# Kernel tuning notes

Measured on AMD Instinct MI355X. Metric: run time of the kernel, lower is better.

## Reference

```python
import jax, jax.numpy as jnp
import numpy as np

EPS = 1e-12  # F.normalize default eps

def _l2_normalize(v):
    # torch.nn.functional.normalize: v / max(||v||_2, eps)
    n = jnp.sqrt(jnp.sum(v * v, axis=-1, keepdims=True))
    return v / jnp.maximum(n, EPS)

def setup_inputs() -> dict:
    key = jax.random.key(0)
    k1, k2 = jax.random.split(key)
    B, M, D = 4096, 12893, 2048
    x = jax.random.normal(k1, (B, D), dtype=jnp.float32)
    prototypes = jax.random.normal(k2, (M, D), dtype=jnp.float32)
    distance_scale = jnp.ones((1,), dtype=jnp.float32)
    return {"x": x, "prototypes": prototypes, "distance_scale": distance_scale}

def reference(x, prototypes, distance_scale):
    xn = _l2_normalize(x)            # [B, D]
    pn = _l2_normalize(prototypes)   # [M, D]
    # pairwise Euclidean distance via ||a||^2 + ||b||^2 - 2 a.b (stable clamp)
    xs = jnp.sum(xn * xn, axis=-1, keepdims=True)        # [B, 1]
    ps = jnp.sum(pn * pn, axis=-1)[None, :]              # [1, M]
    d2 = xs + ps - 2.0 * jnp.einsum('bd,md->bm', xn, pn)  # [B, M]
    dist = jnp.sqrt(jnp.maximum(d2, 0.0))
    x3 = -jnp.abs(distance_scale[0]) * dist              # [B, M]
    # original forward returns (x3, x3, x3, x3); all identical
    return x3
```

## Files before the change

kernel.cpp:

```cpp
#include <hip/hip_runtime.h>
#include <hip/hip_bf16.h>
#include <cstdint>
#include <cstddef>

constexpr int BROWS = 4096;
constexpr int MREAL = 12893;
constexpr int MPAD  = 12928;
constexpr int KDIM  = 2048;

typedef __attribute__((ext_vector_type(8))) short short8;
typedef __attribute__((ext_vector_type(4))) float f32x4;

__device__ __forceinline__ void gld_lds16(const void* g, void* l) {
  __builtin_amdgcn_global_load_lds((__attribute__((address_space(1))) const void*)g,
                                   (__attribute__((address_space(3))) void*)l,
                                   16, 0, 0);
}

__global__ void l2norm_bf16(const float* __restrict__ in,
                            __hip_bfloat16* __restrict__ out,
                            int nvalid) {
  const int row = blockIdx.x;
  const int t   = threadIdx.x;
  __hip_bfloat16* orow = out + (size_t)row * KDIM;

  if (row >= nvalid) {
    reinterpret_cast<float4*>(orow)[t] = make_float4(0.f, 0.f, 0.f, 0.f);
    return;
  }

  const float4* irow = reinterpret_cast<const float4*>(in + (size_t)row * KDIM);
  float4 a = irow[t];
  float4 b = irow[t + 256];
  float ss = a.x*a.x + a.y*a.y + a.z*a.z + a.w*a.w
           + b.x*b.x + b.y*b.y + b.z*b.z + b.w*b.w;

  #pragma unroll
  for (int off = 32; off > 0; off >>= 1) ss += __shfl_down(ss, off);

  __shared__ float red[4];
  if ((t & 63) == 0) red[t >> 6] = ss;
  __syncthreads();
  float tot = red[0] + red[1] + red[2] + red[3];
  float inv = 1.0f / fmaxf(sqrtf(tot), 1e-12f);

  union { ushort4 u; __hip_bfloat16 h[4]; } o1, o2;
  o1.h[0] = __float2bfloat16(a.x * inv);
  o1.h[1] = __float2bfloat16(a.y * inv);
  o1.h[2] = __float2bfloat16(a.z * inv);
  o1.h[3] = __float2bfloat16(a.w * inv);
  o2.h[0] = __float2bfloat16(b.x * inv);
  o2.h[1] = __float2bfloat16(b.y * inv);
  o2.h[2] = __float2bfloat16(b.z * inv);
  o2.h[3] = __float2bfloat16(b.w * inv);
  reinterpret_cast<ushort4*>(orow)[t]       = o1.u;
  reinterpret_cast<ushort4*>(orow)[t + 256] = o2.u;
}

__global__ void gemm_dist(const __hip_bfloat16* __restrict__ A,
                          const __hip_bfloat16* __restrict__ P,
                          const float* __restrict__ scale,
                          float* __restrict__ out) {
  __shared__ __hip_bfloat16 sA[128][32];
  __shared__ __hip_bfloat16 sB[128][32];

  const int tid  = threadIdx.x;
  const int lane = tid & 63;
  const int wave = tid >> 6;
  const int wm   = wave >> 1;
  const int wn   = wave & 1;
  const int bm0  = blockIdx.y * 128;
  const int bn0  = blockIdx.x * 128;

  f32x4 acc[4][4];
  #pragma unroll
  for (int i = 0; i < 4; i++)
    #pragma unroll
    for (int j = 0; j < 4; j++)
      acc[i][j] = f32x4{0.f, 0.f, 0.f, 0.f};

  const int sr = tid >> 2;
  const int sc = (tid & 3) << 3;

  const int frow = lane & 15;
  const int koff = (lane >> 4) << 3;

  for (int kt = 0; kt < KDIM; kt += 32) {
    __syncthreads();
    gld_lds16(A + (size_t)(bm0 + sr)      * KDIM + kt + sc, &sA[sr][sc]);
    gld_lds16(A + (size_t)(bm0 + sr + 64) * KDIM + kt + sc, &sA[sr + 64][sc]);
    gld_lds16(P + (size_t)(bn0 + sr)      * KDIM + kt + sc, &sB[sr][sc]);
    gld_lds16(P + (size_t)(bn0 + sr + 64) * KDIM + kt + sc, &sB[sr + 64][sc]);
    __syncthreads();

    short8 af[4], bf[4];
    #pragma unroll
    for (int i = 0; i < 4; i++)
      af[i] = *reinterpret_cast<const short8*>(&sA[wm * 64 + i * 16 + frow][koff]);
    #pragma unroll
    for (int j = 0; j < 4; j++)
      bf[j] = *reinterpret_cast<const short8*>(&sB[wn * 64 + j * 16 + frow][koff]);

    #pragma unroll
    for (int i = 0; i < 4; i++)
      #pragma unroll
      for (int j = 0; j < 4; j++)
        acc[i][j] = __builtin_amdgcn_mfma_f32_16x16x32_bf16(af[i], bf[j],
                                                            acc[i][j], 0, 0, 0);
  }

  const float s = fabsf(scale[0]);
  const int colb = bn0 + wn * 64 + (lane & 15);
  #pragma unroll
  for (int i = 0; i < 4; i++) {
    const int rowb = bm0 + wm * 64 + i * 16 + ((lane >> 4) << 2);
    #pragma unroll
    for (int j = 0; j < 4; j++) {
      const int col = colb + j * 16;
      if (col < MREAL) {
        #pragma unroll
        for (int r = 0; r < 4; r++) {
          float d2 = fmaxf(2.0f - 2.0f * acc[i][j][r], 0.0f);
          out[(size_t)(rowb + r) * MREAL + col] = -s * __builtin_sqrtf(d2);
        }
      }
    }
  }
}

extern "C" void kernel_launch(void* const* d_in, const int* in_sizes, int n_in,
                              void* d_out, int out_size, void* d_ws, size_t ws_size,
                              hipStream_t stream) {
  const float* x = (const float*)d_in[0];
  const float* p = (const float*)d_in[1];
  const float* s = (const float*)d_in[2];
  float* out = (float*)d_out;

  __hip_bfloat16* xn = (__hip_bfloat16*)d_ws;
  __hip_bfloat16* pn = xn + (size_t)BROWS * KDIM;

  l2norm_bf16<<<BROWS, 256, 0, stream>>>(x, xn, BROWS);
  l2norm_bf16<<<MPAD,  256, 0, stream>>>(p, pn, MREAL);

  dim3 grid(MPAD / 128, BROWS / 128);
  gemm_dist<<<grid, 256, 0, stream>>>(xn, pn, s, out);
}
```

Measured before the change: 635.8 us.

## Rewrite GEMM with 256x256 tiles, double-buffered swizzled LDS pipeline, fused normalization

The GEMM now uses 512-thread blocks computing 256x256 output tiles with a K-step of 64. Operands go through double-buffered, XOR-swizzled LDS fed by async global-to-LDS loads, staged across four sub-phases per tile with explicit waitcnt, barriers and setprio. Blocks are remapped with an XCD-aware swizzle over a 1D grid, and the two normalization launches are merged into one. This aims to cut LDS and global traffic per FLOP and to hide load latency, in exchange for much higher register and LDS pressure and a fragile hand-written schedule.

```diff
diff --git a/kernel.cpp b/kernel.cpp
--- a/kernel.cpp
+++ b/kernel.cpp
@@ -7,6 +7,7 @@
 constexpr int MREAL = 12893;
 constexpr int MPAD  = 12928;
 constexpr int KDIM  = 2048;
+constexpr int NT    = KDIM / 64;
 
 typedef __attribute__((ext_vector_type(8))) short short8;
 typedef __attribute__((ext_vector_type(4))) float f32x4;
@@ -17,23 +18,32 @@
                                    16, 0, 0);
 }
 
-__global__ void l2norm_bf16(const float* __restrict__ in,
-                            __hip_bfloat16* __restrict__ out,
-                            int nvalid) {
-  const int row = blockIdx.x;
-  const int t   = threadIdx.x;
-  __hip_bfloat16* orow = out + (size_t)row * KDIM;
-
-  if (row >= nvalid) {
-    reinterpret_cast<float4*>(orow)[t] = make_float4(0.f, 0.f, 0.f, 0.f);
-    return;
-  }
-
-  const float4* irow = reinterpret_cast<const float4*>(in + (size_t)row * KDIM);
-  float4 a = irow[t];
-  float4 b = irow[t + 256];
+__global__ void l2norm_fused(const float* __restrict__ x,
+                             const float* __restrict__ p,
+                             __hip_bfloat16* __restrict__ xn,
+                             __hip_bfloat16* __restrict__ pn) {
+  const int b = blockIdx.x;
+  const int t = threadIdx.x;
+  const float* irow;
+  __hip_bfloat16* orow;
+  if (b < BROWS) {
+    irow = x + (size_t)b * KDIM;
+    orow = xn + (size_t)b * KDIM;
+  } else {
+    const int row = b - BROWS;
+    orow = pn + (size_t)row * KDIM;
+    if (row >= MREAL) {
+      reinterpret_cast<float4*>(orow)[t] = make_float4(0.f, 0.f, 0.f, 0.f);
+      return;
+    }
+    irow = p + (size_t)row * KDIM;
+  }
+
+  const float4* iv = reinterpret_cast<const float4*>(irow);
+  float4 a = iv[t];
+  float4 c = iv[t + 256];
   float ss = a.x*a.x + a.y*a.y + a.z*a.z + a.w*a.w
-           + b.x*b.x + b.y*b.y + b.z*b.z + b.w*b.w;
+           + c.x*c.x + c.y*c.y + c.z*c.z + c.w*c.w;
 
   #pragma unroll
   for (int off = 32; off > 0; off >>= 1) ss += __shfl_down(ss, off);
@@ -49,84 +59,142 @@
   o1.h[1] = __float2bfloat16(a.y * inv);
   o1.h[2] = __float2bfloat16(a.z * inv);
   o1.h[3] = __float2bfloat16(a.w * inv);
-  o2.h[0] = __float2bfloat16(b.x * inv);
-  o2.h[1] = __float2bfloat16(b.y * inv);
-  o2.h[2] = __float2bfloat16(b.z * inv);
-  o2.h[3] = __float2bfloat16(b.w * inv);
+  o2.h[0] = __float2bfloat16(c.x * inv);
+  o2.h[1] = __float2bfloat16(c.y * inv);
+  o2.h[2] = __float2bfloat16(c.z * inv);
+  o2.h[3] = __float2bfloat16(c.w * inv);
   reinterpret_cast<ushort4*>(orow)[t]       = o1.u;
   reinterpret_cast<ushort4*>(orow)[t + 256] = o2.u;
 }
 
-__global__ void gemm_dist(const __hip_bfloat16* __restrict__ A,
-                          const __hip_bfloat16* __restrict__ P,
-                          const float* __restrict__ scale,
-                          float* __restrict__ out) {
-  __shared__ __hip_bfloat16 sA[128][32];
-  __shared__ __hip_bfloat16 sB[128][32];
-
-  const int tid  = threadIdx.x;
-  const int lane = tid & 63;
-  const int wave = tid >> 6;
-  const int wm   = wave >> 1;
-  const int wn   = wave & 1;
-  const int bm0  = blockIdx.y * 128;
-  const int bn0  = blockIdx.x * 128;
-
-  f32x4 acc[4][4];
-  #pragma unroll
-  for (int i = 0; i < 4; i++)
+__global__ __launch_bounds__(512, 2)
+void gemm_dist(const __hip_bfloat16* __restrict__ A,
+               const __hip_bfloat16* __restrict__ P,
+               const float* __restrict__ scale,
+               float* __restrict__ out) {
+  __shared__ __hip_bfloat16 lds[65536];
+  __hip_bfloat16* const sA = lds;
+  __hip_bfloat16* const sB = lds + 32768;
+
+  const int t    = threadIdx.x;
+  const int lane = t & 63;
+  const int wv   = t >> 6;
+  const int wm   = wv >> 2;
+  const int wn   = wv & 3;
+
+  const int bid = blockIdx.x;
+  const int swz = (bid & 7) * 102 + (bid >> 3);
+  const int bm0 = (swz / 51) * 256;
+  const int bn0 = (swz % 51) * 256;
+
+  const int srow = t >> 3;
+  const int sp   = t & 7;
+  const int ssl  = sp ^ (srow & 7);
+  const __hip_bfloat16* aSrc[4];
+  const __hip_bfloat16* bSrc[4];
+  int sOff[4];
+  #pragma unroll
+  for (int r = 0; r < 4; ++r) {
+    aSrc[r] = A + (size_t)(bm0 + r*64 + srow) * KDIM + ssl*8;
+    int br = bn0 + r*64 + srow;
+    br = br < MPAD ? br : (MPAD - 1);
+    bSrc[r] = P + (size_t)br * KDIM + ssl*8;
+    sOff[r] = (r*64 + srow)*64 + sp*8;
+  }
+
+  const int l15 = lane & 15, hi = lane >> 4;
+  const int pk0 = ( hi      ^ (lane & 7)) * 8;
+  const int pk1 = ((hi + 4) ^ (lane & 7)) * 8;
+  const int aBase = (wm*128 + l15) * 64;
+  const int bBase = (wn*64  + l15) * 64;
+
+  f32x4 acc[8][4];
+  #pragma unroll
+  for (int i = 0; i < 8; ++i)
     #pragma unroll
-    for (int j = 0; j < 4; j++)
-      acc[i][j] = f32x4{0.f, 0.f, 0.f, 0.f};
-
-  const int sr = tid >> 2;
-  const int sc = (tid & 3) << 3;
-
-  const int frow = lane & 15;
-  const int koff = (lane >> 4) << 3;
-
-  for (int kt = 0; kt < KDIM; kt += 32) {
-    __syncthreads();
-    gld_lds16(A + (size_t)(bm0 + sr)      * KDIM + kt + sc, &sA[sr][sc]);
-    gld_lds16(A + (size_t)(bm0 + sr + 64) * KDIM + kt + sc, &sA[sr + 64][sc]);
-    gld_lds16(P + (size_t)(bn0 + sr)      * KDIM + kt + sc, &sB[sr][sc]);
-    gld_lds16(P + (size_t)(bn0 + sr + 64) * KDIM + kt + sc, &sB[sr + 64][sc]);
-    __syncthreads();
-
-    short8 af[4], bf[4];
+    for (int j = 0; j < 4; ++j) acc[i][j] = f32x4{0.f, 0.f, 0.f, 0.f};
+
+#define STG_A(BUF, R, T) do { const int kt_ = ((T)*64) & (KDIM-1);            \
+    gld_lds16(aSrc[(R)]   + kt_, sA + (BUF)*16384 + sOff[(R)]);               \
+    gld_lds16(aSrc[(R)+1] + kt_, sA + (BUF)*16384 + sOff[(R)+1]); } while(0)
+#define STG_B(BUF, R, T) do { const int kt_ = ((T)*64) & (KDIM-1);            \
+    gld_lds16(bSrc[(R)]   + kt_, sB + (BUF)*16384 + sOff[(R)]);               \
+    gld_lds16(bSrc[(R)+1] + kt_, sB + (BUF)*16384 + sOff[(R)+1]); } while(0)
+
+  STG_A(0, 0, 0); STG_A(0, 2, 0);
+  STG_B(0, 0, 0); STG_B(0, 2, 0);
+  STG_B(1, 0, 1); STG_B(1, 2, 1);
+  asm volatile("s_waitcnt vmcnt(4)" ::: "memory");
+  __builtin_amdgcn_s_barrier();
+
+  short8 bfr[4][2];
+
+#define PHASE(BUF, Q, READB, STG, VM) do {                                    \
+    asm volatile("" ::: "memory");                                            \
+    const __hip_bfloat16* sAb = sA + (BUF)*16384;                             \
+    const __hip_bfloat16* sBb = sB + (BUF)*16384;                             \
+    if (READB) {                                                              \
+      _Pragma("unroll")                                                       \
+      for (int j = 0; j < 4; ++j) {                                           \
+        bfr[j][0] = *reinterpret_cast<const short8*>(sBb + bBase + j*1024 + pk0); \
+        bfr[j][1] = *reinterpret_cast<const short8*>(sBb + bBase + j*1024 + pk1); \
+      }                                                                       \
+    }                                                                         \
+    const short8 a00 = *reinterpret_cast<const short8*>(sAb + aBase + (Q)*2048 + pk0); \
+    const short8 a01 = *reinterpret_cast<const short8*>(sAb + aBase + (Q)*2048 + pk1); \
+    const short8 a10 = *reinterpret_cast<const short8*>(sAb + aBase + (Q)*2048 + 1024 + pk0); \
+    const short8 a11 = *reinterpret_cast<const short8*>(sAb + aBase + (Q)*2048 + 1024 + pk1); \
+    STG;                                                                      \
+    __builtin_amdgcn_s_barrier();                                             \
+    asm volatile("s_waitcnt lgkmcnt(0)" ::: "memory");                        \
+    __builtin_amdgcn_s_setprio(1);                                            \
+    _Pragma("unroll")                                                         \
+    for (int j = 0; j < 4; ++j) {                                             \
+      acc[2*(Q)  ][j] = __builtin_amdgcn_mfma_f32_16x16x32_bf16(a00, bfr[j][0], acc[2*(Q)  ][j], 0, 0, 0); \
+      acc[2*(Q)  ][j] = __builtin_amdgcn_mfma_f32_16x16x32_bf16(a01, bfr[j][1], acc[2*(Q)  ][j], 0, 0, 0); \
+      acc[2*(Q)+1][j] = __builtin_amdgcn_mfma_f32_16x16x32_bf16(a10, bfr[j][0], acc[2*(Q)+1][j], 0, 0, 0); \
+      acc[2*(Q)+1][j] = __builtin_amdgcn_mfma_f32_16x16x32_bf16(a11, bfr[j][1], acc[2*(Q)+1][j], 0, 0, 0); \
+    }                                                                         \
+    __builtin_amdgcn_s_setprio(0);                                            \
+    if (VM) asm volatile("s_waitcnt vmcnt(4)" ::: "memory");                  \
+    __builtin_amdgcn_s_barrier();                                             \
+  } while (0)
+
+  for (int it = 0; it < NT/2; ++it) {
+    const int T1 = 2*it + 1;
+    PHASE(0, 0, true , STG_A(1, 0, T1),     false);
+    PHASE(0, 1, false, STG_A(1, 2, T1),     false);
+    PHASE(0, 2, false, STG_B(0, 0, (T1+1)), false);
+    PHASE(0, 3, false, STG_B(0, 2, (T1+1)), true );
+    PHASE(1, 0, true , STG_A(0, 0, (T1+1)), false);
+    PHASE(1, 1, false, STG_A(0, 2, (T1+1)), false);
+    PHASE(1, 2, false, STG_B(1, 0, (T1+2)), false);
+    PHASE(1, 3, false, STG_B(1, 2, (T1+2)), true );
+  }
+
+  const float s = fabsf(scale[0]);
+  const int colb = bn0 + wn*64 + l15;
+  #pragma unroll
+  for (int i = 0; i < 8; ++i) {
+    const int rowb = bm0 + wm*128 + i*16 + hi*4;
     #pragma unroll
-    for (int i = 0; i < 4; i++)
-      af[i] = *reinterpret_cast<const short8*>(&sA[wm * 64 + i * 16 + frow][koff]);
-    #pragma unroll
-    for (int j = 0; j < 4; j++)
-      bf[j] = *reinterpret_cast<const short8*>(&sB[wn * 64 + j * 16 + frow][koff]);
-
-    #pragma unroll
-    for (int i = 0; i < 4; i++)
-      #pragma unroll
-      for (int j = 0; j < 4; j++)
-        acc[i][j] = __builtin_amdgcn_mfma_f32_16x16x32_bf16(af[i], bf[j],
-                                                            acc[i][j], 0, 0, 0);
-  }
-
-  const float s = fabsf(scale[0]);
-  const int colb = bn0 + wn * 64 + (lane & 15);
-  #pragma unroll
-  for (int i = 0; i < 4; i++) {
-    const int rowb = bm0 + wm * 64 + i * 16 + ((lane >> 4) << 2);
-    #pragma unroll
-    for (int j = 0; j < 4; j++) {
-      const int col = colb + j * 16;
+    for (int j = 0; j < 4; ++j) {
+      const int col = colb + j*16;
       if (col < MREAL) {
         #pragma unroll
-        for (int r = 0; r < 4; r++) {
-          float d2 = fmaxf(2.0f - 2.0f * acc[i][j][r], 0.0f);
-          out[(size_t)(rowb + r) * MREAL + col] = -s * __builtin_sqrtf(d2);
+        for (int r = 0; r < 4; ++r) {
+          float d2 = fmaxf(2.0f - 2.0f*acc[i][j][r], 0.0f);
+          out[(size_t)(rowb + r)*MREAL + col] = -s * __builtin_sqrtf(d2);
         }
       }
     }
   }
-}
+  asm volatile("s_waitcnt vmcnt(0)" ::: "memory");
+}
+
+#undef PHASE
+#undef STG_A
+#undef STG_B
 
 extern "C" void kernel_launch(void* const* d_in, const int* in_sizes, int n_in,
                               void* d_out, int out_size, void* d_ws, size_t ws_size,
@@ -139,9 +207,7 @@
   __hip_bfloat16* xn = (__hip_bfloat16*)d_ws;
   __hip_bfloat16* pn = xn + (size_t)BROWS * KDIM;
 
-  l2norm_bf16<<<BROWS, 256, 0, stream>>>(x, xn, BROWS);
-  l2norm_bf16<<<MPAD,  256, 0, stream>>>(p, pn, MREAL);
-
-  dim3 grid(MPAD / 128, BROWS / 128);
-  gemm_dist<<<grid, 256, 0, stream>>>(xn, pn, s, out);
-}
+  l2norm_fused<<<BROWS + MPAD, 256, 0, stream>>>(x, p, xn, pn);
+
+  gemm_dist<<<816, 512, 0, stream>>>(xn, pn, s, out);
+}
```

Measured after the change: 522.6 us. 17.8% less time.
